# Kernel tuning notes

Hardware: AMD Instinct MI355X
Metric: run time of the kernel (lower is better)

The kernel has to match this reference:

```python
import jax, jax.numpy as jnp
import numpy as np

D_MODEL = 1024
NUM_HEADS = 16
HEAD_DIM = D_MODEL // NUM_HEADS
ROPE_BASE = 10000.0


def setup_inputs() -> dict:
    key = jax.random.key(0)
    ks = jax.random.split(key, 9)
    B, S = 2, 2048
    x = jax.random.normal(ks[0], (B, S, D_MODEL), dtype=jnp.float32)
    s = 1.0 / np.sqrt(D_MODEL)
    Wq = jax.random.normal(ks[1], (D_MODEL, D_MODEL), dtype=jnp.float32) * s
    bq = jnp.zeros((D_MODEL,), dtype=jnp.float32)
    Wk = jax.random.normal(ks[2], (D_MODEL, D_MODEL), dtype=jnp.float32) * s
    bk = jnp.zeros((D_MODEL,), dtype=jnp.float32)
    Wv = jax.random.normal(ks[3], (D_MODEL, D_MODEL), dtype=jnp.float32) * s
    bv = jnp.zeros((D_MODEL,), dtype=jnp.float32)
    Wo = jax.random.normal(ks[4], (D_MODEL, D_MODEL), dtype=jnp.float32) * s
    bo = jnp.zeros((D_MODEL,), dtype=jnp.float32)
    return {"x": x, "Wq": Wq, "bq": bq, "Wk": Wk, "bk": bk,
            "Wv": Wv, "bv": bv, "Wo": Wo, "bo": bo}


def _apply_rope(x):
    # x: [B, H, S, Dh]; interleaved complex-pair RoPE (torch.view_as_complex style)
    B, H, S, Dh = x.shape
    inv_freq = 1.0 / (ROPE_BASE ** (jnp.arange(0, Dh, 2, dtype=jnp.float32) / Dh))
    pos = jnp.arange(S, dtype=jnp.float32)
    freqs = pos[:, None] * inv_freq[None, :]            # [S, Dh/2]
    cos, sin = jnp.cos(freqs), jnp.sin(freqs)           # each [S, Dh/2]
    x2 = x.reshape(B, H, S, Dh // 2, 2)
    xr, xi = x2[..., 0], x2[..., 1]
    out_r = xr * cos - xi * sin
    out_i = xr * sin + xi * cos
    return jnp.stack([out_r, out_i], axis=-1).reshape(B, H, S, Dh)


def reference(x, Wq, bq, Wk, bk, Wv, bv, Wo, bo):
    B, S, _ = x.shape
    H, Dh = NUM_HEADS, HEAD_DIM
    def proj(W, b):
        y = jnp.einsum('bsd,ed->bse', x, W) + b          # torch Linear: x @ W.T + b
        return y.reshape(B, S, H, Dh).transpose(0, 2, 1, 3)  # [B,H,S,Dh]
    Q = _apply_rope(proj(Wq, bq))
    K = _apply_rope(proj(Wk, bk))
    V = proj(Wv, bv)
    scale = 1.0 / jnp.sqrt(jnp.float32(Dh))
    scores = jnp.einsum('bhqd,bhkd->bhqk', Q, K) * scale
    causal = jnp.tril(jnp.ones((S, S), dtype=bool))
    scores = jnp.where(causal, scores, jnp.float32(-jnp.inf))
    attn = jax.nn.softmax(scores, axis=-1)
    out = jnp.einsum('bhqk,bhkd->bhqd', attn, V)         # [B,H,S,Dh]
    out = out.transpose(0, 2, 1, 3).reshape(B, S, H * Dh)
    return jnp.einsum('bsd,ed->bse', out, Wo) + bo
```

## Files before the change

### kernel.cpp

```cpp
#include <hip/hip_runtime.h>
#include <stdint.h>

#define S_LEN 2048
#define BATCH 2
#define DM 1024
#define NH 16
#define DH 64
#define MROWS 4096

typedef unsigned short u16;
typedef unsigned int u32;
typedef __attribute__((ext_vector_type(8))) short bf16x8;
typedef __attribute__((ext_vector_type(4))) float f32x4;
typedef __attribute__((ext_vector_type(2))) unsigned u32x2;

union pack8 { u32 w[4]; bf16x8 v8; };

__device__ inline u16 f2bf(float f) {
  union { float f; unsigned u; } v; v.f = f;
  unsigned u = v.u;
  unsigned r = u + 0x7fffu + ((u >> 16) & 1u);
  return (u16)(r >> 16);
}

__device__ inline u32 pkbf(float lo, float hi) {
  u32 r;
  asm("v_cvt_pk_bf16_f32 %0, %1, %2" : "=v"(r) : "v"(lo), "v"(hi));
  return r;
}

__device__ inline float bf2f(short s) {
  union { u32 u; float f; } c; c.u = ((u32)(u16)s) << 16;
  return c.f;
}

__global__ void convert_k(const float* __restrict__ x, const float* __restrict__ wq,
                          const float* __restrict__ wk, const float* __restrict__ wv,
                          const float* __restrict__ wo, u16* __restrict__ xb,
                          u16* __restrict__ wb) {
  int i = blockIdx.x * blockDim.x + threadIdx.x;
  const int total = (MROWS * DM + 4 * DM * DM) / 4;
  if (i >= total) return;
  int e = i * 4;
  const float* src;
  u16* dst;
  if (e < MROWS * DM) {
    src = x + e; dst = xb + e;
  } else {
    int j = e - MROWS * DM;
    int w = j >> 20;
    int o = j & ((1 << 20) - 1);
    src = (w == 0) ? wq + o : (w == 1) ? wk + o : (w == 2) ? wv + o : wo + o;
    dst = wb + j;
  }
  float4 v = *(const float4*)src;
  uint2 r;
  r.x = (unsigned)f2bf(v.x) | ((unsigned)f2bf(v.y) << 16);
  r.y = (unsigned)f2bf(v.z) | ((unsigned)f2bf(v.w) << 16);
  *(uint2*)dst = r;
}

__global__ void rope_k(float2* __restrict__ tab, float* __restrict__ kmax) {
  int i = blockIdx.x * blockDim.x + threadIdx.x;
  if (i < 32) kmax[i] = 0.f;
  if (i >= S_LEN * 32) return;
  int s = i >> 5, p = i & 31;
  float inv = expf(-(float)p * 0.28782313662425575f);
  float a = (float)s * inv;
  tab[i] = make_float2(cosf(a), sinf(a));
}

__global__ void knorm_k(const u16* __restrict__ K, float* __restrict__ kmax) {
  const int row = blockIdx.x * 256 + threadIdx.x;
  const int bh = row >> 11;
  const u16* p = K + (size_t)row * DH;
  float ss = 0.f;
#pragma unroll
  for (int i = 0; i < 8; i++) {
    bf16x8 v = *(const bf16x8*)(p + i * 8);
#pragma unroll
    for (int j = 0; j < 8; j++) { float f = bf2f(v[j]); ss += f * f; }
  }
  float kn = sqrtf(ss);
#pragma unroll
  for (int d = 1; d < 64; d <<= 1) kn = fmaxf(kn, __shfl_xor(kn, d));
  if ((threadIdx.x & 63) == 0)
    atomicMax((unsigned*)(kmax + bh), __float_as_uint(kn));
}

__launch_bounds__(256)
__global__ void gemm_k(const u16* __restrict__ A,
                       const u16* __restrict__ w0, const u16* __restrict__ w1,
                       const u16* __restrict__ w2,
                       const float* __restrict__ b0, const float* __restrict__ b1,
                       const float* __restrict__ b2,
                       const float2* __restrict__ rope,
                       void* __restrict__ o0, void* __restrict__ o1, void* __restrict__ o2,
                       int mode0) {
  const int mode = mode0 + (int)(blockIdx.x >> 8);
  const int tile = blockIdx.x & 255;
  const int mt = tile >> 3, nt = tile & 7;
  const int mbase = mt * 128, nbase = nt * 128;
  const u16* W = (mode == 1) ? w1 : (mode == 2) ? w2 : w0;
  const float* bias = (mode == 1) ? b1 : (mode == 2) ? b2 : b0;
  void* outp = (mode == 1) ? o1 : (mode == 2) ? o2 : o0;

  __shared__ u16 As[128 * 40];
  __shared__ u16 Bs[128 * 40];

  const int t = threadIdx.x;
  const int lane = t & 63, wvi = t >> 6;
  const int lr = lane & 15, lg = lane >> 4;
  const int wm = (wvi >> 1) * 64, wn = (wvi & 1) * 64;

  f32x4 acc[4][4] = {};
  const int srow = t >> 2;
  const int scol = (t & 3) * 8;

  for (int kk = 0; kk < DM; kk += 32) {
    bf16x8 a0 = *(const bf16x8*)(A + (size_t)(mbase + srow) * DM + kk + scol);
    bf16x8 a1 = *(const bf16x8*)(A + (size_t)(mbase + 64 + srow) * DM + kk + scol);
    bf16x8 g0 = *(const bf16x8*)(W + (size_t)(nbase + srow) * DM + kk + scol);
    bf16x8 g1 = *(const bf16x8*)(W + (size_t)(nbase + 64 + srow) * DM + kk + scol);
    __syncthreads();
    *(bf16x8*)&As[srow * 40 + scol] = a0;
    *(bf16x8*)&As[(64 + srow) * 40 + scol] = a1;
    *(bf16x8*)&Bs[srow * 40 + scol] = g0;
    *(bf16x8*)&Bs[(64 + srow) * 40 + scol] = g1;
    __syncthreads();
    bf16x8 af[4], bfr[4];
#pragma unroll
    for (int mi = 0; mi < 4; mi++)
      af[mi] = *(const bf16x8*)&As[(wm + mi * 16 + lr) * 40 + lg * 8];
#pragma unroll
    for (int ni = 0; ni < 4; ni++)
      bfr[ni] = *(const bf16x8*)&Bs[(wn + ni * 16 + lr) * 40 + lg * 8];
#pragma unroll
    for (int mi = 0; mi < 4; mi++)
#pragma unroll
      for (int ni = 0; ni < 4; ni++)
        acc[mi][ni] = __builtin_amdgcn_mfma_f32_16x16x32_bf16(af[mi], bfr[ni], acc[mi][ni], 0, 0, 0);
  }

#pragma unroll
  for (int ni = 0; ni < 4; ni++) {
    const int col = nbase + wn + ni * 16 + lr;
    const float bv = bias[col];
#pragma unroll
    for (int mi = 0; mi < 4; mi++) {
      const int row0 = mbase + wm + mi * 16 + lg * 4;
      f32x4 v = acc[mi][ni];
#pragma unroll
      for (int r = 0; r < 4; r++) {
        float val = v[r] + bv;
        const int row = row0 + r;
        if (mode <= 1) {
          float nb = __shfl_xor(val, 1);
          const int d = col & 63, p = d >> 1, s = row & (S_LEN - 1);
          float2 cs = rope[s * 32 + p];
          float ov = (d & 1) ? (nb * cs.y + val * cs.x) : (val * cs.x - nb * cs.y);
          if (mode == 0) ov *= 0.18033688011112042f;
          const int b = row >> 11, h = col >> 6;
          ((u16*)outp)[((size_t)(b * NH + h) * S_LEN + s) * DH + d] = f2bf(ov);
        } else if (mode == 2) {
          const int b = row >> 11, h = col >> 6, d = col & 63, s = row & (S_LEN - 1);
          const int j = s & 31;
          const int pos = (s & ~31) + (((j & 15) >> 2) << 3) + ((j >> 4) << 2) + (j & 3);
          ((u16*)outp)[((size_t)(b * NH + h) * DH + d) * S_LEN + pos] = f2bf(val);
        } else {
          ((float*)outp)[(size_t)row * DM + col] = val;
        }
      }
    }
  }
}

__device__ __forceinline__ void sm_pv_static(const float a[8], float m, float& l,
                                             bf16x8 v0, bf16x8 v1, bf16x8 v2, bf16x8 v3,
                                             f32x4* o) {
  float p[8];
#pragma unroll
  for (int r = 0; r < 8; r++) p[r] = __builtin_amdgcn_exp2f(a[r] - m);
  l += ((p[0] + p[1]) + (p[2] + p[3])) + ((p[4] + p[5]) + (p[6] + p[7]));
  pack8 pu;
  pu.w[0] = pkbf(p[0], p[1]);
  pu.w[1] = pkbf(p[2], p[3]);
  pu.w[2] = pkbf(p[4], p[5]);
  pu.w[3] = pkbf(p[6], p[7]);
  o[0] = __builtin_amdgcn_mfma_f32_16x16x32_bf16(v0, pu.v8, o[0], 0, 0, 0);
  o[2] = __builtin_amdgcn_mfma_f32_16x16x32_bf16(v1, pu.v8, o[2], 0, 0, 0);
  o[4] = __builtin_amdgcn_mfma_f32_16x16x32_bf16(v2, pu.v8, o[4], 0, 0, 0);
  o[6] = __builtin_amdgcn_mfma_f32_16x16x32_bf16(v3, pu.v8, o[6], 0, 0, 0);
}

__launch_bounds__(64)
__global__ void attn_k(const u16* __restrict__ Q, const u16* __restrict__ K,
                       const u16* __restrict__ Vt, u16* __restrict__ Oo,
                       const float* __restrict__ kmax) {
  const int bh = blockIdx.x & 31;
  const int tile = 63 - (blockIdx.x >> 5);
  const int qbase = tile * 32;
  const int lane = threadIdx.x;
  const int lr = lane & 15, lg = lane >> 4;

  const size_t qoff = ((size_t)bh * S_LEN + qbase + lr) * DH + lg * 8;
  const bf16x8 qA0 = *(const bf16x8*)(Q + qoff);
  const bf16x8 qA1 = *(const bf16x8*)(Q + qoff + 32);
  const bf16x8 qB0 = *(const bf16x8*)(Q + qoff + 16 * DH);
  const bf16x8 qB1 = *(const bf16x8*)(Q + qoff + 16 * DH + 32);

  float ssA = 0.f, ssB = 0.f;
#pragma unroll
  for (int j = 0; j < 8; j++) {
    float a0 = bf2f(qA0[j]), a1 = bf2f(qA1[j]);
    float b0 = bf2f(qB0[j]), b1 = bf2f(qB1[j]);
    ssA += a0 * a0 + a1 * a1;
    ssB += b0 * b0 + b1 * b1;
  }
  ssA += __shfl_xor(ssA, 16); ssA += __shfl_xor(ssA, 32);
  ssB += __shfl_xor(ssB, 16); ssB += __shfl_xor(ssB, 32);
  const float kmx = kmax[bh];
  const float mA = sqrtf(ssA) * kmx;
  const float mB = sqrtf(ssB) * kmx;

  f32x4 o[8] = {};
  float lA = 0.f, lB = 0.f;
  const f32x4 zero = {};
  const int nst = tile + 1;

  const u16* Kp = K + ((size_t)bh * S_LEN + lr) * DH + lg * 8;
  const u16* Vp = Vt + ((size_t)bh * DH + lr) * S_LEN + lg * 8;
  bf16x8 kc0 = *(const bf16x8*)(Kp);
  bf16x8 kc1 = *(const bf16x8*)(Kp + 32);
  bf16x8 kc2 = *(const bf16x8*)(Kp + 16 * DH);
  bf16x8 kc3 = *(const bf16x8*)(Kp + 16 * DH + 32);

  for (int it = 0; it < nst - 1; ++it) {
    bf16x8 v0 = *(const bf16x8*)(Vp);
    bf16x8 v1 = *(const bf16x8*)(Vp + 16 * S_LEN);
    bf16x8 v2 = *(const bf16x8*)(Vp + 32 * S_LEN);
    bf16x8 v3 = *(const bf16x8*)(Vp + 48 * S_LEN);
    Vp += 32;

    f32x4 sA0 = __builtin_amdgcn_mfma_f32_16x16x32_bf16(kc0, qA0, zero, 0, 0, 0);
    sA0 = __builtin_amdgcn_mfma_f32_16x16x32_bf16(kc1, qA1, sA0, 0, 0, 0);
    f32x4 sA1 = __builtin_amdgcn_mfma_f32_16x16x32_bf16(kc2, qA0, zero, 0, 0, 0);
    sA1 = __builtin_amdgcn_mfma_f32_16x16x32_bf16(kc3, qA1, sA1, 0, 0, 0);
    f32x4 sB0 = __builtin_amdgcn_mfma_f32_16x16x32_bf16(kc0, qB0, zero, 0, 0, 0);
    sB0 = __builtin_amdgcn_mfma_f32_16x16x32_bf16(kc1, qB1, sB0, 0, 0, 0);
    f32x4 sB1 = __builtin_amdgcn_mfma_f32_16x16x32_bf16(kc2, qB0, zero, 0, 0, 0);
    sB1 = __builtin_amdgcn_mfma_f32_16x16x32_bf16(kc3, qB1, sB1, 0, 0, 0);

    Kp += 32 * DH;
    kc0 = *(const bf16x8*)(Kp);
    kc1 = *(const bf16x8*)(Kp + 32);
    kc2 = *(const bf16x8*)(Kp + 16 * DH);
    kc3 = *(const bf16x8*)(Kp + 16 * DH + 32);

    float aA[8], aB[8];
#pragma unroll
    for (int r = 0; r < 4; r++) {
      aA[r] = sA0[r]; aA[4 + r] = sA1[r];
      aB[r] = sB0[r]; aB[4 + r] = sB1[r];
    }
    sm_pv_static(aA, mA, lA, v0, v1, v2, v3, &o[0]);
    sm_pv_static(aB, mB, lB, v0, v1, v2, v3, &o[1]);
  }

  {
    bf16x8 v0 = *(const bf16x8*)(Vp);
    bf16x8 v1 = *(const bf16x8*)(Vp + 16 * S_LEN);
    bf16x8 v2 = *(const bf16x8*)(Vp + 32 * S_LEN);
    bf16x8 v3 = *(const bf16x8*)(Vp + 48 * S_LEN);

    f32x4 sA0 = __builtin_amdgcn_mfma_f32_16x16x32_bf16(kc0, qA0, zero, 0, 0, 0);
    sA0 = __builtin_amdgcn_mfma_f32_16x16x32_bf16(kc1, qA1, sA0, 0, 0, 0);
    f32x4 sA1 = __builtin_amdgcn_mfma_f32_16x16x32_bf16(kc2, qA0, zero, 0, 0, 0);
    sA1 = __builtin_amdgcn_mfma_f32_16x16x32_bf16(kc3, qA1, sA1, 0, 0, 0);
    f32x4 sB0 = __builtin_amdgcn_mfma_f32_16x16x32_bf16(kc0, qB0, zero, 0, 0, 0);
    sB0 = __builtin_amdgcn_mfma_f32_16x16x32_bf16(kc1, qB1, sB0, 0, 0, 0);
    f32x4 sB1 = __builtin_amdgcn_mfma_f32_16x16x32_bf16(kc2, qB0, zero, 0, 0, 0);
    sB1 = __builtin_amdgcn_mfma_f32_16x16x32_bf16(kc3, qB1, sB1, 0, 0, 0);

    const int qrelA = lr - lg * 4;
    const int qrelB = qrelA + 16;
    float aA[8], aB[8];
#pragma unroll
    for (int r = 0; r < 4; r++) {
      aA[r]     = (r <= qrelA)      ? sA0[r] : -__builtin_inff();
      aA[4 + r] = (r + 16 <= qrelA) ? sA1[r] : -__builtin_inff();
      aB[r]     = sB0[r];
      aB[4 + r] = (r + 16 <= qrelB) ? sB1[r] : -__builtin_inff();
    }
    sm_pv_static(aA, mA, lA, v0, v1, v2, v3, &o[0]);
    sm_pv_static(aB, mB, lB, v0, v1, v2, v3, &o[1]);
  }

  lA += __shfl_xor(lA, 16); lA += __shfl_xor(lA, 32);
  lB += __shfl_xor(lB, 16); lB += __shfl_xor(lB, 32);
  const float rlA = __builtin_amdgcn_rcpf(lA);
  const float rlB = __builtin_amdgcn_rcpf(lB);

  const int b = bh >> 4, h = bh & 15;
  const size_t obaseA = ((size_t)b * S_LEN + qbase + lr) * DM + h * DH;
  const size_t obaseB = obaseA + (size_t)16 * DM;
#pragma unroll
  for (int dt = 0; dt < 4; dt++) {
    u32x2 pkA, pkB;
    pkA.x = pkbf(o[dt * 2][0] * rlA, o[dt * 2][1] * rlA);
    pkA.y = pkbf(o[dt * 2][2] * rlA, o[dt * 2][3] * rlA);
    pkB.x = pkbf(o[dt * 2 + 1][0] * rlB, o[dt * 2 + 1][1] * rlB);
    pkB.y = pkbf(o[dt * 2 + 1][2] * rlB, o[dt * 2 + 1][3] * rlB);
    *(u32x2*)(Oo + obaseA + dt * 16 + lg * 4) = pkA;
    *(u32x2*)(Oo + obaseB + dt * 16 + lg * 4) = pkB;
  }
}

extern "C" void kernel_launch(void* const* d_in, const int* in_sizes, int n_in,
                              void* d_out, int out_size, void* d_ws, size_t ws_size,
                              hipStream_t stream) {
  const float* x  = (const float*)d_in[0];
  const float* Wq = (const float*)d_in[1];
  const float* bq = (const float*)d_in[2];
  const float* Wk = (const float*)d_in[3];
  const float* bk = (const float*)d_in[4];
  const float* Wv = (const float*)d_in[5];
  const float* bv = (const float*)d_in[6];
  const float* Wo = (const float*)d_in[7];
  const float* bo = (const float*)d_in[8];

  char* ws = (char*)d_ws;
  u16* xb    = (u16*)(ws);
  u16* wb    = (u16*)(ws + (8u << 20));
  u16* Qb    = (u16*)(ws + (16u << 20));
  u16* Kb    = (u16*)(ws + (24u << 20));
  u16* Vtb   = (u16*)(ws + (32u << 20));
  u16* AOb   = (u16*)(ws + (40u << 20));
  float2* rt = (float2*)(ws + (48u << 20));
  float* kmx = (float*)(ws + (48u << 20) + (512u << 10));

  convert_k<<<8192, 256, 0, stream>>>(x, Wq, Wk, Wv, Wo, xb, wb);
  rope_k<<<256, 256, 0, stream>>>(rt, kmx);
  gemm_k<<<768, 256, 0, stream>>>(xb, wb, wb + (1u << 20), wb + (2u << 20),
                                  bq, bk, bv, rt, Qb, Kb, Vtb, 0);
  knorm_k<<<256, 256, 0, stream>>>(Kb, kmx);
  attn_k<<<2048, 64, 0, stream>>>(Qb, Kb, Vtb, AOb, kmx);
  gemm_k<<<256, 256, 0, stream>>>(AOb, wb + (3u << 20), wb + (3u << 20), wb + (3u << 20),
                                  bo, bo, bo, rt, d_out, d_out, d_out, 3);
}
```

Baseline: 171.1 us.

## Split attention into 16-row query tiles with two interleaved KV streams

The attention kernel now handles 16 query rows per wavefront instead of 32 and launches twice as many blocks. Each wavefront walks two independent halves of the causal key range at once, each with its own accumulators, and combines them at the end. This relies on the static-max softmax (a bound from query norm times max key norm), so no rescaling is needed when merging. The goal is more parallelism, better load balance and more independent MFMA/load chains to hide latency, at the cost of reading K/V twice as often per query row.

```diff
diff --git a/kernel.cpp b/kernel.cpp
--- a/kernel.cpp
+++ b/kernel.cpp
@@ -175,9 +175,9 @@
   }
 }
 
-__device__ __forceinline__ void sm_pv_static(const float a[8], float m, float& l,
-                                             bf16x8 v0, bf16x8 v1, bf16x8 v2, bf16x8 v3,
-                                             f32x4* o) {
+__device__ __forceinline__ void sm_pv(const float a[8], float m, float& l,
+                                      bf16x8 v0, bf16x8 v1, bf16x8 v2, bf16x8 v3,
+                                      f32x4* o) {
   float p[8];
 #pragma unroll
   for (int r = 0; r < 8; r++) p[r] = __builtin_amdgcn_exp2f(a[r] - m);
@@ -188,9 +188,9 @@
   pu.w[2] = pkbf(p[4], p[5]);
   pu.w[3] = pkbf(p[6], p[7]);
   o[0] = __builtin_amdgcn_mfma_f32_16x16x32_bf16(v0, pu.v8, o[0], 0, 0, 0);
-  o[2] = __builtin_amdgcn_mfma_f32_16x16x32_bf16(v1, pu.v8, o[2], 0, 0, 0);
-  o[4] = __builtin_amdgcn_mfma_f32_16x16x32_bf16(v2, pu.v8, o[4], 0, 0, 0);
-  o[6] = __builtin_amdgcn_mfma_f32_16x16x32_bf16(v3, pu.v8, o[6], 0, 0, 0);
+  o[1] = __builtin_amdgcn_mfma_f32_16x16x32_bf16(v1, pu.v8, o[1], 0, 0, 0);
+  o[2] = __builtin_amdgcn_mfma_f32_16x16x32_bf16(v2, pu.v8, o[2], 0, 0, 0);
+  o[3] = __builtin_amdgcn_mfma_f32_16x16x32_bf16(v3, pu.v8, o[3], 0, 0, 0);
 }
 
 __launch_bounds__(64)
@@ -198,121 +198,137 @@
                        const u16* __restrict__ Vt, u16* __restrict__ Oo,
                        const float* __restrict__ kmax) {
   const int bh = blockIdx.x & 31;
-  const int tile = 63 - (blockIdx.x >> 5);
-  const int qbase = tile * 32;
+  const int tile = blockIdx.x >> 5;
+  const int qbase = tile * 16;
   const int lane = threadIdx.x;
   const int lr = lane & 15, lg = lane >> 4;
 
   const size_t qoff = ((size_t)bh * S_LEN + qbase + lr) * DH + lg * 8;
-  const bf16x8 qA0 = *(const bf16x8*)(Q + qoff);
-  const bf16x8 qA1 = *(const bf16x8*)(Q + qoff + 32);
-  const bf16x8 qB0 = *(const bf16x8*)(Q + qoff + 16 * DH);
-  const bf16x8 qB1 = *(const bf16x8*)(Q + qoff + 16 * DH + 32);
-
-  float ssA = 0.f, ssB = 0.f;
+  const bf16x8 q0 = *(const bf16x8*)(Q + qoff);
+  const bf16x8 q1 = *(const bf16x8*)(Q + qoff + 32);
+
+  float ss = 0.f;
 #pragma unroll
   for (int j = 0; j < 8; j++) {
-    float a0 = bf2f(qA0[j]), a1 = bf2f(qA1[j]);
-    float b0 = bf2f(qB0[j]), b1 = bf2f(qB1[j]);
-    ssA += a0 * a0 + a1 * a1;
-    ssB += b0 * b0 + b1 * b1;
-  }
-  ssA += __shfl_xor(ssA, 16); ssA += __shfl_xor(ssA, 32);
-  ssB += __shfl_xor(ssB, 16); ssB += __shfl_xor(ssB, 32);
-  const float kmx = kmax[bh];
-  const float mA = sqrtf(ssA) * kmx;
-  const float mB = sqrtf(ssB) * kmx;
-
-  f32x4 o[8] = {};
-  float lA = 0.f, lB = 0.f;
+    float a0 = bf2f(q0[j]), a1 = bf2f(q1[j]);
+    ss += a0 * a0 + a1 * a1;
+  }
+  ss += __shfl_xor(ss, 16); ss += __shfl_xor(ss, 32);
+  const float m = sqrtf(ss) * kmax[bh];
+
+  f32x4 o0[4] = {}, o1[4] = {};
+  float l0 = 0.f, l1 = 0.f;
   const f32x4 zero = {};
-  const int nst = tile + 1;
-
-  const u16* Kp = K + ((size_t)bh * S_LEN + lr) * DH + lg * 8;
-  const u16* Vp = Vt + ((size_t)bh * DH + lr) * S_LEN + lg * 8;
-  bf16x8 kc0 = *(const bf16x8*)(Kp);
-  bf16x8 kc1 = *(const bf16x8*)(Kp + 32);
-  bf16x8 kc2 = *(const bf16x8*)(Kp + 16 * DH);
-  bf16x8 kc3 = *(const bf16x8*)(Kp + 16 * DH + 32);
-
-  for (int it = 0; it < nst - 1; ++it) {
-    bf16x8 v0 = *(const bf16x8*)(Vp);
-    bf16x8 v1 = *(const bf16x8*)(Vp + 16 * S_LEN);
-    bf16x8 v2 = *(const bf16x8*)(Vp + 32 * S_LEN);
-    bf16x8 v3 = *(const bf16x8*)(Vp + 48 * S_LEN);
-    Vp += 32;
-
-    f32x4 sA0 = __builtin_amdgcn_mfma_f32_16x16x32_bf16(kc0, qA0, zero, 0, 0, 0);
-    sA0 = __builtin_amdgcn_mfma_f32_16x16x32_bf16(kc1, qA1, sA0, 0, 0, 0);
-    f32x4 sA1 = __builtin_amdgcn_mfma_f32_16x16x32_bf16(kc2, qA0, zero, 0, 0, 0);
-    sA1 = __builtin_amdgcn_mfma_f32_16x16x32_bf16(kc3, qA1, sA1, 0, 0, 0);
-    f32x4 sB0 = __builtin_amdgcn_mfma_f32_16x16x32_bf16(kc0, qB0, zero, 0, 0, 0);
-    sB0 = __builtin_amdgcn_mfma_f32_16x16x32_bf16(kc1, qB1, sB0, 0, 0, 0);
-    f32x4 sB1 = __builtin_amdgcn_mfma_f32_16x16x32_bf16(kc2, qB0, zero, 0, 0, 0);
-    sB1 = __builtin_amdgcn_mfma_f32_16x16x32_bf16(kc3, qB1, sB1, 0, 0, 0);
-
-    Kp += 32 * DH;
-    kc0 = *(const bf16x8*)(Kp);
-    kc1 = *(const bf16x8*)(Kp + 32);
-    kc2 = *(const bf16x8*)(Kp + 16 * DH);
-    kc3 = *(const bf16x8*)(Kp + 16 * DH + 32);
-
-    float aA[8], aB[8];
+  const int nst = (qbase + 47) >> 5;
+  const int half = nst >> 1;
+  const int jn = (nst - 1) >> 1;
+  const int solo = half - jn;
+
+  const u16* Kp0 = K + ((size_t)bh * S_LEN + lr) * DH + lg * 8;
+  const u16* Kp1 = K + ((size_t)bh * S_LEN + half * 32 + lr) * DH + lg * 8;
+  const u16* Vp0 = Vt + ((size_t)bh * DH + lr) * S_LEN + lg * 8;
+  const u16* Vp1 = Vp0 + half * 32;
+
+  bf16x8 kc00 = *(const bf16x8*)(Kp0);
+  bf16x8 kc01 = *(const bf16x8*)(Kp0 + 32);
+  bf16x8 kc02 = *(const bf16x8*)(Kp0 + 16 * DH);
+  bf16x8 kc03 = *(const bf16x8*)(Kp0 + 16 * DH + 32);
+  bf16x8 kc10 = *(const bf16x8*)(Kp1);
+  bf16x8 kc11 = *(const bf16x8*)(Kp1 + 32);
+  bf16x8 kc12 = *(const bf16x8*)(Kp1 + 16 * DH);
+  bf16x8 kc13 = *(const bf16x8*)(Kp1 + 16 * DH + 32);
+
+  for (int it = 0; it < jn; ++it) {
+    bf16x8 va0 = *(const bf16x8*)(Vp0);
+    bf16x8 va1 = *(const bf16x8*)(Vp0 + 16 * S_LEN);
+    bf16x8 va2 = *(const bf16x8*)(Vp0 + 32 * S_LEN);
+    bf16x8 va3 = *(const bf16x8*)(Vp0 + 48 * S_LEN);
+    bf16x8 vb0 = *(const bf16x8*)(Vp1);
+    bf16x8 vb1 = *(const bf16x8*)(Vp1 + 16 * S_LEN);
+    bf16x8 vb2 = *(const bf16x8*)(Vp1 + 32 * S_LEN);
+    bf16x8 vb3 = *(const bf16x8*)(Vp1 + 48 * S_LEN);
+    Vp0 += 32; Vp1 += 32;
+
+    f32x4 sa0 = __builtin_amdgcn_mfma_f32_16x16x32_bf16(kc00, q0, zero, 0, 0, 0);
+    sa0 = __builtin_amdgcn_mfma_f32_16x16x32_bf16(kc01, q1, sa0, 0, 0, 0);
+    f32x4 sa1 = __builtin_amdgcn_mfma_f32_16x16x32_bf16(kc02, q0, zero, 0, 0, 0);
+    sa1 = __builtin_amdgcn_mfma_f32_16x16x32_bf16(kc03, q1, sa1, 0, 0, 0);
+    f32x4 sb0 = __builtin_amdgcn_mfma_f32_16x16x32_bf16(kc10, q0, zero, 0, 0, 0);
+    sb0 = __builtin_amdgcn_mfma_f32_16x16x32_bf16(kc11, q1, sb0, 0, 0, 0);
+    f32x4 sb1 = __builtin_amdgcn_mfma_f32_16x16x32_bf16(kc12, q0, zero, 0, 0, 0);
+    sb1 = __builtin_amdgcn_mfma_f32_16x16x32_bf16(kc13, q1, sb1, 0, 0, 0);
+
+    Kp0 += 32 * DH;
+    kc00 = *(const bf16x8*)(Kp0);
+    kc01 = *(const bf16x8*)(Kp0 + 32);
+    kc02 = *(const bf16x8*)(Kp0 + 16 * DH);
+    kc03 = *(const bf16x8*)(Kp0 + 16 * DH + 32);
+    Kp1 += 32 * DH;
+    kc10 = *(const bf16x8*)(Kp1);
+    kc11 = *(const bf16x8*)(Kp1 + 32);
+    kc12 = *(const bf16x8*)(Kp1 + 16 * DH);
+    kc13 = *(const bf16x8*)(Kp1 + 16 * DH + 32);
+
+    float aa[8], ab[8];
 #pragma unroll
     for (int r = 0; r < 4; r++) {
-      aA[r] = sA0[r]; aA[4 + r] = sA1[r];
-      aB[r] = sB0[r]; aB[4 + r] = sB1[r];
+      aa[r] = sa0[r]; aa[4 + r] = sa1[r];
+      ab[r] = sb0[r]; ab[4 + r] = sb1[r];
     }
-    sm_pv_static(aA, mA, lA, v0, v1, v2, v3, &o[0]);
-    sm_pv_static(aB, mB, lB, v0, v1, v2, v3, &o[1]);
+    sm_pv(aa, m, l0, va0, va1, va2, va3, o0);
+    sm_pv(ab, m, l1, vb0, vb1, vb2, vb3, o1);
+  }
+
+  if (solo) {
+    bf16x8 va0 = *(const bf16x8*)(Vp0);
+    bf16x8 va1 = *(const bf16x8*)(Vp0 + 16 * S_LEN);
+    bf16x8 va2 = *(const bf16x8*)(Vp0 + 32 * S_LEN);
+    bf16x8 va3 = *(const bf16x8*)(Vp0 + 48 * S_LEN);
+
+    f32x4 sa0 = __builtin_amdgcn_mfma_f32_16x16x32_bf16(kc00, q0, zero, 0, 0, 0);
+    sa0 = __builtin_amdgcn_mfma_f32_16x16x32_bf16(kc01, q1, sa0, 0, 0, 0);
+    f32x4 sa1 = __builtin_amdgcn_mfma_f32_16x16x32_bf16(kc02, q0, zero, 0, 0, 0);
+    sa1 = __builtin_amdgcn_mfma_f32_16x16x32_bf16(kc03, q1, sa1, 0, 0, 0);
+
+    float aa[8];
+#pragma unroll
+    for (int r = 0; r < 4; r++) { aa[r] = sa0[r]; aa[4 + r] = sa1[r]; }
+    sm_pv(aa, m, l0, va0, va1, va2, va3, o0);
   }
 
   {
-    bf16x8 v0 = *(const bf16x8*)(Vp);
-    bf16x8 v1 = *(const bf16x8*)(Vp + 16 * S_LEN);
-    bf16x8 v2 = *(const bf16x8*)(Vp + 32 * S_LEN);
-    bf16x8 v3 = *(const bf16x8*)(Vp + 48 * S_LEN);
-
-    f32x4 sA0 = __builtin_amdgcn_mfma_f32_16x16x32_bf16(kc0, qA0, zero, 0, 0, 0);
-    sA0 = __builtin_amdgcn_mfma_f32_16x16x32_bf16(kc1, qA1, sA0, 0, 0, 0);
-    f32x4 sA1 = __builtin_amdgcn_mfma_f32_16x16x32_bf16(kc2, qA0, zero, 0, 0, 0);
-    sA1 = __builtin_amdgcn_mfma_f32_16x16x32_bf16(kc3, qA1, sA1, 0, 0, 0);
-    f32x4 sB0 = __builtin_amdgcn_mfma_f32_16x16x32_bf16(kc0, qB0, zero, 0, 0, 0);
-    sB0 = __builtin_amdgcn_mfma_f32_16x16x32_bf16(kc1, qB1, sB0, 0, 0, 0);
-    f32x4 sB1 = __builtin_amdgcn_mfma_f32_16x16x32_bf16(kc2, qB0, zero, 0, 0, 0);
-    sB1 = __builtin_amdgcn_mfma_f32_16x16x32_bf16(kc3, qB1, sB1, 0, 0, 0);
-
-    const int qrelA = lr - lg * 4;
-    const int qrelB = qrelA + 16;
-    float aA[8], aB[8];
+    bf16x8 vb0 = *(const bf16x8*)(Vp1);
+    bf16x8 vb1 = *(const bf16x8*)(Vp1 + 16 * S_LEN);
+    bf16x8 vb2 = *(const bf16x8*)(Vp1 + 32 * S_LEN);
+    bf16x8 vb3 = *(const bf16x8*)(Vp1 + 48 * S_LEN);
+
+    f32x4 sb0 = __builtin_amdgcn_mfma_f32_16x16x32_bf16(kc10, q0, zero, 0, 0, 0);
+    sb0 = __builtin_amdgcn_mfma_f32_16x16x32_bf16(kc11, q1, sb0, 0, 0, 0);
+    f32x4 sb1 = __builtin_amdgcn_mfma_f32_16x16x32_bf16(kc12, q0, zero, 0, 0, 0);
+    sb1 = __builtin_amdgcn_mfma_f32_16x16x32_bf16(kc13, q1, sb1, 0, 0, 0);
+
+    const int qrel = qbase + lr - (nst - 1) * 32 - lg * 4;
+    float ab[8];
 #pragma unroll
     for (int r = 0; r < 4; r++) {
-      aA[r]     = (r <= qrelA)      ? sA0[r] : -__builtin_inff();
-      aA[4 + r] = (r + 16 <= qrelA) ? sA1[r] : -__builtin_inff();
-      aB[r]     = sB0[r];
-      aB[4 + r] = (r + 16 <= qrelB) ? sB1[r] : -__builtin_inff();
+      ab[r]     = (r <= qrel)      ? sb0[r] : -__builtin_inff();
+      ab[4 + r] = (r + 16 <= qrel) ? sb1[r] : -__builtin_inff();
     }
-    sm_pv_static(aA, mA, lA, v0, v1, v2, v3, &o[0]);
-    sm_pv_static(aB, mB, lB, v0, v1, v2, v3, &o[1]);
-  }
-
-  lA += __shfl_xor(lA, 16); lA += __shfl_xor(lA, 32);
-  lB += __shfl_xor(lB, 16); lB += __shfl_xor(lB, 32);
-  const float rlA = __builtin_amdgcn_rcpf(lA);
-  const float rlB = __builtin_amdgcn_rcpf(lB);
+    sm_pv(ab, m, l1, vb0, vb1, vb2, vb3, o1);
+  }
+
+  float l = l0 + l1;
+  l += __shfl_xor(l, 16); l += __shfl_xor(l, 32);
+  const float rl = __builtin_amdgcn_rcpf(l);
 
   const int b = bh >> 4, h = bh & 15;
-  const size_t obaseA = ((size_t)b * S_LEN + qbase + lr) * DM + h * DH;
-  const size_t obaseB = obaseA + (size_t)16 * DM;
+  const size_t obase = ((size_t)b * S_LEN + qbase + lr) * DM + h * DH;
 #pragma unroll
   for (int dt = 0; dt < 4; dt++) {
-    u32x2 pkA, pkB;
-    pkA.x = pkbf(o[dt * 2][0] * rlA, o[dt * 2][1] * rlA);
-    pkA.y = pkbf(o[dt * 2][2] * rlA, o[dt * 2][3] * rlA);
-    pkB.x = pkbf(o[dt * 2 + 1][0] * rlB, o[dt * 2 + 1][1] * rlB);
-    pkB.y = pkbf(o[dt * 2 + 1][2] * rlB, o[dt * 2 + 1][3] * rlB);
-    *(u32x2*)(Oo + obaseA + dt * 16 + lg * 4) = pkA;
-    *(u32x2*)(Oo + obaseB + dt * 16 + lg * 4) = pkB;
+    u32x2 pk;
+    pk.x = pkbf((o0[dt][0] + o1[dt][0]) * rl, (o0[dt][1] + o1[dt][1]) * rl);
+    pk.y = pkbf((o0[dt][2] + o1[dt][2]) * rl, (o0[dt][3] + o1[dt][3]) * rl);
+    *(u32x2*)(Oo + obase + dt * 16 + lg * 4) = pk;
   }
 }
 
@@ -344,7 +360,7 @@
   gemm_k<<<768, 256, 0, stream>>>(xb, wb, wb + (1u << 20), wb + (2u << 20),
                                   bq, bk, bv, rt, Qb, Kb, Vtb, 0);
   knorm_k<<<256, 256, 0, stream>>>(Kb, kmx);
-  attn_k<<<2048, 64, 0, stream>>>(Qb, Kb, Vtb, AOb, kmx);
+  attn_k<<<4096, 64, 0, stream>>>(Qb, Kb, Vtb, AOb, kmx);
   gemm_k<<<256, 256, 0, stream>>>(AOb, wb + (3u << 20), wb + (3u << 20), wb + (3u << 20),
                                   bo, bo, bo, rt, d_out, d_out, d_out, 3);
 }
```

New measurement: 227.6 us. 33.0% more time.

## Share K/V tiles across four waves via double-buffered LDS in attention

Applied to the files above, without the earlier changes.

The attention kernel moves from one wave per 32-query tile to 256-thread blocks, where four waves handle four consecutive query tiles. Each 32-key K/V chunk is loaded once per block with global_load_lds into swizzled, double-buffered shared memory, and the next chunk is prefetched while the current one is computed. This cuts redundant global and L2 loads of K and V. In exchange, every step now pays two block barriers and applies the causal mask on every iteration. Lower-index waves also run up to three extra fully masked iterations, because all waves loop to the block's last tile.

```diff
diff --git a/kernel.cpp b/kernel.cpp
--- a/kernel.cpp
+++ b/kernel.cpp
@@ -32,6 +32,12 @@
 __device__ inline float bf2f(short s) {
   union { u32 u; float f; } c; c.u = ((u32)(u16)s) << 16;
   return c.f;
+}
+
+__device__ __forceinline__ void gload_lds16(const u16* g, u16* l) {
+  __builtin_amdgcn_global_load_lds(
+      (const __attribute__((address_space(1))) u32*)g,
+      (__attribute__((address_space(3))) u32*)l, 16, 0, 0);
 }
 
 __global__ void convert_k(const float* __restrict__ x, const float* __restrict__ wq,
@@ -175,9 +181,9 @@
   }
 }
 
-__device__ __forceinline__ void sm_pv_static(const float a[8], float m, float& l,
-                                             bf16x8 v0, bf16x8 v1, bf16x8 v2, bf16x8 v3,
-                                             f32x4* o) {
+__device__ __forceinline__ void sm_pv(const float a[8], float m, float& l,
+                                      bf16x8 v0, bf16x8 v1, bf16x8 v2, bf16x8 v3,
+                                      f32x4* o) {
   float p[8];
 #pragma unroll
   for (int r = 0; r < 8; r++) p[r] = __builtin_amdgcn_exp2f(a[r] - m);
@@ -188,20 +194,35 @@
   pu.w[2] = pkbf(p[4], p[5]);
   pu.w[3] = pkbf(p[6], p[7]);
   o[0] = __builtin_amdgcn_mfma_f32_16x16x32_bf16(v0, pu.v8, o[0], 0, 0, 0);
-  o[2] = __builtin_amdgcn_mfma_f32_16x16x32_bf16(v1, pu.v8, o[2], 0, 0, 0);
-  o[4] = __builtin_amdgcn_mfma_f32_16x16x32_bf16(v2, pu.v8, o[4], 0, 0, 0);
-  o[6] = __builtin_amdgcn_mfma_f32_16x16x32_bf16(v3, pu.v8, o[6], 0, 0, 0);
-}
-
-__launch_bounds__(64)
+  o[1] = __builtin_amdgcn_mfma_f32_16x16x32_bf16(v1, pu.v8, o[1], 0, 0, 0);
+  o[2] = __builtin_amdgcn_mfma_f32_16x16x32_bf16(v2, pu.v8, o[2], 0, 0, 0);
+  o[3] = __builtin_amdgcn_mfma_f32_16x16x32_bf16(v3, pu.v8, o[3], 0, 0, 0);
+}
+
+__launch_bounds__(256)
 __global__ void attn_k(const u16* __restrict__ Q, const u16* __restrict__ K,
                        const u16* __restrict__ Vt, u16* __restrict__ Oo,
                        const float* __restrict__ kmax) {
   const int bh = blockIdx.x & 31;
-  const int tile = 63 - (blockIdx.x >> 5);
+  const int g = 15 - (int)(blockIdx.x >> 5);
+  const int tid = threadIdx.x;
+  const int w = tid >> 6;
+  const int lane = tid & 63;
+  const int lr = lane & 15, lg = lane >> 4;
+  const int tile = g * 4 + w;
   const int qbase = tile * 32;
-  const int lane = threadIdx.x;
-  const int lr = lane & 15, lg = lane >> 4;
+  const int nst = g * 4 + 4;
+
+  __shared__ u16 Ks[2][2048];
+  __shared__ u16 Vs[2][2048];
+
+  const u16* Kg = K + (size_t)bh * S_LEN * DH;
+  const u16* Vg = Vt + (size_t)bh * DH * S_LEN;
+
+  const int kr = tid >> 3, kcB = (tid & 7) << 4;
+  const int vr = tid >> 2, vcB = (tid & 3) << 4;
+  const int ksrcoff = ((kcB ^ ((kr & 7) << 4)) >> 1);
+  const int vsrcoff = ((vcB ^ ((vr & 3) << 4)) >> 1);
 
   const size_t qoff = ((size_t)bh * S_LEN + qbase + lr) * DH + lg * 8;
   const bf16x8 qA0 = *(const bf16x8*)(Q + qoff);
@@ -223,77 +244,63 @@
   const float mA = sqrtf(ssA) * kmx;
   const float mB = sqrtf(ssB) * kmx;
 
-  f32x4 o[8] = {};
+  f32x4 oA[4] = {}, oB[4] = {};
   float lA = 0.f, lB = 0.f;
   const f32x4 zero = {};
-  const int nst = tile + 1;
-
-  const u16* Kp = K + ((size_t)bh * S_LEN + lr) * DH + lg * 8;
-  const u16* Vp = Vt + ((size_t)bh * DH + lr) * S_LEN + lg * 8;
-  bf16x8 kc0 = *(const bf16x8*)(Kp);
-  bf16x8 kc1 = *(const bf16x8*)(Kp + 32);
-  bf16x8 kc2 = *(const bf16x8*)(Kp + 16 * DH);
-  bf16x8 kc3 = *(const bf16x8*)(Kp + 16 * DH + 32);
-
-  for (int it = 0; it < nst - 1; ++it) {
-    bf16x8 v0 = *(const bf16x8*)(Vp);
-    bf16x8 v1 = *(const bf16x8*)(Vp + 16 * S_LEN);
-    bf16x8 v2 = *(const bf16x8*)(Vp + 32 * S_LEN);
-    bf16x8 v3 = *(const bf16x8*)(Vp + 48 * S_LEN);
-    Vp += 32;
-
-    f32x4 sA0 = __builtin_amdgcn_mfma_f32_16x16x32_bf16(kc0, qA0, zero, 0, 0, 0);
-    sA0 = __builtin_amdgcn_mfma_f32_16x16x32_bf16(kc1, qA1, sA0, 0, 0, 0);
-    f32x4 sA1 = __builtin_amdgcn_mfma_f32_16x16x32_bf16(kc2, qA0, zero, 0, 0, 0);
-    sA1 = __builtin_amdgcn_mfma_f32_16x16x32_bf16(kc3, qA1, sA1, 0, 0, 0);
-    f32x4 sB0 = __builtin_amdgcn_mfma_f32_16x16x32_bf16(kc0, qB0, zero, 0, 0, 0);
-    sB0 = __builtin_amdgcn_mfma_f32_16x16x32_bf16(kc1, qB1, sB0, 0, 0, 0);
-    f32x4 sB1 = __builtin_amdgcn_mfma_f32_16x16x32_bf16(kc2, qB0, zero, 0, 0, 0);
-    sB1 = __builtin_amdgcn_mfma_f32_16x16x32_bf16(kc3, qB1, sB1, 0, 0, 0);
-
-    Kp += 32 * DH;
-    kc0 = *(const bf16x8*)(Kp);
-    kc1 = *(const bf16x8*)(Kp + 32);
-    kc2 = *(const bf16x8*)(Kp + 16 * DH);
-    kc3 = *(const bf16x8*)(Kp + 16 * DH + 32);
-
-    float aA[8], aB[8];
-#pragma unroll
-    for (int r = 0; r < 4; r++) {
-      aA[r] = sA0[r]; aA[4 + r] = sA1[r];
-      aB[r] = sB0[r]; aB[4 + r] = sB1[r];
+
+  const int kmsk = (lr & 7) << 4;
+  const int k00 = lr * 64 + (((lg << 4)) ^ kmsk) / 2;
+  const int k01 = lr * 64 + ((64 + (lg << 4)) ^ kmsk) / 2;
+  const int k10 = (16 + lr) * 64 + (((lg << 4)) ^ kmsk) / 2;
+  const int k11 = (16 + lr) * 64 + ((64 + (lg << 4)) ^ kmsk) / 2;
+  const int vmsk = (lr & 3) << 4;
+  const int vo = ((lg << 4) ^ vmsk) / 2;
+
+  gload_lds16(Kg + (size_t)kr * DH + ksrcoff, &Ks[0][w << 9]);
+  gload_lds16(Vg + (size_t)vr * S_LEN + vsrcoff, &Vs[0][w << 9]);
+
+  for (int s = 0; s < nst; ++s) {
+    const int b = s & 1;
+    if (s + 1 < nst) {
+      gload_lds16(Kg + (size_t)((s + 1) * 32 + kr) * DH + ksrcoff, &Ks[b ^ 1][w << 9]);
+      gload_lds16(Vg + (size_t)vr * S_LEN + (s + 1) * 32 + vsrcoff, &Vs[b ^ 1][w << 9]);
     }
-    sm_pv_static(aA, mA, lA, v0, v1, v2, v3, &o[0]);
-    sm_pv_static(aB, mB, lB, v0, v1, v2, v3, &o[1]);
-  }
-
-  {
-    bf16x8 v0 = *(const bf16x8*)(Vp);
-    bf16x8 v1 = *(const bf16x8*)(Vp + 16 * S_LEN);
-    bf16x8 v2 = *(const bf16x8*)(Vp + 32 * S_LEN);
-    bf16x8 v3 = *(const bf16x8*)(Vp + 48 * S_LEN);
-
-    f32x4 sA0 = __builtin_amdgcn_mfma_f32_16x16x32_bf16(kc0, qA0, zero, 0, 0, 0);
-    sA0 = __builtin_amdgcn_mfma_f32_16x16x32_bf16(kc1, qA1, sA0, 0, 0, 0);
-    f32x4 sA1 = __builtin_amdgcn_mfma_f32_16x16x32_bf16(kc2, qA0, zero, 0, 0, 0);
-    sA1 = __builtin_amdgcn_mfma_f32_16x16x32_bf16(kc3, qA1, sA1, 0, 0, 0);
-    f32x4 sB0 = __builtin_amdgcn_mfma_f32_16x16x32_bf16(kc0, qB0, zero, 0, 0, 0);
-    sB0 = __builtin_amdgcn_mfma_f32_16x16x32_bf16(kc1, qB1, sB0, 0, 0, 0);
-    f32x4 sB1 = __builtin_amdgcn_mfma_f32_16x16x32_bf16(kc2, qB0, zero, 0, 0, 0);
-    sB1 = __builtin_amdgcn_mfma_f32_16x16x32_bf16(kc3, qB1, sB1, 0, 0, 0);
-
-    const int qrelA = lr - lg * 4;
+    __syncthreads();
+
+    const u16* Kb = Ks[b];
+    const u16* Vb = Vs[b];
+    bf16x8 kc0 = *(const bf16x8*)&Kb[k00];
+    bf16x8 kc1 = *(const bf16x8*)&Kb[k01];
+    bf16x8 kc2 = *(const bf16x8*)&Kb[k10];
+    bf16x8 kc3 = *(const bf16x8*)&Kb[k11];
+    bf16x8 v0 = *(const bf16x8*)&Vb[(lr) * 32 + vo];
+    bf16x8 v1 = *(const bf16x8*)&Vb[(16 + lr) * 32 + vo];
+    bf16x8 v2 = *(const bf16x8*)&Vb[(32 + lr) * 32 + vo];
+    bf16x8 v3 = *(const bf16x8*)&Vb[(48 + lr) * 32 + vo];
+
+    f32x4 s0A = __builtin_amdgcn_mfma_f32_16x16x32_bf16(kc0, qA0, zero, 0, 0, 0);
+    s0A = __builtin_amdgcn_mfma_f32_16x16x32_bf16(kc1, qA1, s0A, 0, 0, 0);
+    f32x4 s1A = __builtin_amdgcn_mfma_f32_16x16x32_bf16(kc2, qA0, zero, 0, 0, 0);
+    s1A = __builtin_amdgcn_mfma_f32_16x16x32_bf16(kc3, qA1, s1A, 0, 0, 0);
+    f32x4 s0B = __builtin_amdgcn_mfma_f32_16x16x32_bf16(kc0, qB0, zero, 0, 0, 0);
+    s0B = __builtin_amdgcn_mfma_f32_16x16x32_bf16(kc1, qB1, s0B, 0, 0, 0);
+    f32x4 s1B = __builtin_amdgcn_mfma_f32_16x16x32_bf16(kc2, qB0, zero, 0, 0, 0);
+    s1B = __builtin_amdgcn_mfma_f32_16x16x32_bf16(kc3, qB1, s1B, 0, 0, 0);
+
+    const int qrelA = qbase + lr - (s << 5) - (lg << 2);
     const int qrelB = qrelA + 16;
     float aA[8], aB[8];
 #pragma unroll
     for (int r = 0; r < 4; r++) {
-      aA[r]     = (r <= qrelA)      ? sA0[r] : -__builtin_inff();
-      aA[4 + r] = (r + 16 <= qrelA) ? sA1[r] : -__builtin_inff();
-      aB[r]     = sB0[r];
-      aB[4 + r] = (r + 16 <= qrelB) ? sB1[r] : -__builtin_inff();
+      aA[r]     = (r <= qrelA)      ? s0A[r] : -__builtin_inff();
+      aA[4 + r] = (r + 16 <= qrelA) ? s1A[r] : -__builtin_inff();
+      aB[r]     = (r <= qrelB)      ? s0B[r] : -__builtin_inff();
+      aB[4 + r] = (r + 16 <= qrelB) ? s1B[r] : -__builtin_inff();
     }
-    sm_pv_static(aA, mA, lA, v0, v1, v2, v3, &o[0]);
-    sm_pv_static(aB, mB, lB, v0, v1, v2, v3, &o[1]);
+    sm_pv(aA, mA, lA, v0, v1, v2, v3, oA);
+    sm_pv(aB, mB, lB, v0, v1, v2, v3, oB);
+
+    __syncthreads();
   }
 
   lA += __shfl_xor(lA, 16); lA += __shfl_xor(lA, 32);
@@ -301,16 +308,16 @@
   const float rlA = __builtin_amdgcn_rcpf(lA);
   const float rlB = __builtin_amdgcn_rcpf(lB);
 
-  const int b = bh >> 4, h = bh & 15;
-  const size_t obaseA = ((size_t)b * S_LEN + qbase + lr) * DM + h * DH;
+  const int bb = bh >> 4, h = bh & 15;
+  const size_t obaseA = ((size_t)bb * S_LEN + qbase + lr) * DM + h * DH;
   const size_t obaseB = obaseA + (size_t)16 * DM;
 #pragma unroll
   for (int dt = 0; dt < 4; dt++) {
     u32x2 pkA, pkB;
-    pkA.x = pkbf(o[dt * 2][0] * rlA, o[dt * 2][1] * rlA);
-    pkA.y = pkbf(o[dt * 2][2] * rlA, o[dt * 2][3] * rlA);
-    pkB.x = pkbf(o[dt * 2 + 1][0] * rlB, o[dt * 2 + 1][1] * rlB);
-    pkB.y = pkbf(o[dt * 2 + 1][2] * rlB, o[dt * 2 + 1][3] * rlB);
+    pkA.x = pkbf(oA[dt][0] * rlA, oA[dt][1] * rlA);
+    pkA.y = pkbf(oA[dt][2] * rlA, oA[dt][3] * rlA);
+    pkB.x = pkbf(oB[dt][0] * rlB, oB[dt][1] * rlB);
+    pkB.y = pkbf(oB[dt][2] * rlB, oB[dt][3] * rlB);
     *(u32x2*)(Oo + obaseA + dt * 16 + lg * 4) = pkA;
     *(u32x2*)(Oo + obaseB + dt * 16 + lg * 4) = pkB;
   }
@@ -344,7 +351,7 @@
   gemm_k<<<768, 256, 0, stream>>>(xb, wb, wb + (1u << 20), wb + (2u << 20),
                                   bq, bk, bv, rt, Qb, Kb, Vtb, 0);
   knorm_k<<<256, 256, 0, stream>>>(Kb, kmx);
-  attn_k<<<2048, 64, 0, stream>>>(Qb, Kb, Vtb, AOb, kmx);
+  attn_k<<<512, 256, 0, stream>>>(Qb, Kb, Vtb, AOb, kmx);
   gemm_k<<<256, 256, 0, stream>>>(AOb, wb + (3u << 20), wb + (3u << 20), wb + (3u << 20),
                                   bo, bo, bo, rt, d_out, d_out, d_out, 3);
 }
```

New measurement: 158.0 us. 1.08x faster.
